# Kernel tuning notes

Hardware: AMD Instinct MI355X
Metric: run time of the kernel (lower is better)

The kernel has to match this reference:

```python
import jax, jax.numpy as jnp
import numpy as np

EPS = 1e-5
NEG_SLOPE = 0.2

def _layernorm(x, g, b):
    mu = x.mean(-1, keepdims=True)
    var = ((x - mu) ** 2).mean(-1, keepdims=True)
    return (x - mu) * jax.lax.rsqrt(var + EPS) * g + b

def _forward(h, edge_attr, rel_emb, W_l, b_l, W_r, b_r, W_e, att, bias, gate,
             g1, bt1, g2, bt2, Wf1, bf1, Wf2, bf2, edge_index, edge_type):
    N, F = h.shape
    R, H, C = att.shape
    HC = H * C
    E = edge_type.shape[0]
    De = edge_attr.shape[1]
    src, dst = edge_index[0], edge_index[1]

    # per-relation GATv2 linear projections: lin_l / lin_r  -> [N, R, H*C]
    xl = jnp.einsum('nf,rfh->nrh', h, W_l) + b_l
    xr = jnp.einsum('nf,rfh->nrh', h, W_r) + b_r
    # gather per edge using its own relation's weights
    xl_e = xl[src, edge_type]          # [E, HC]  (source, lin_l)
    xr_e = xr[dst, edge_type]          # [E, HC]  (dest,  lin_r)

    # edge features: lin_edge over concat([edge_attr, rel_emb[r]]) with per-relation weights
    e_feat = jnp.zeros((E, HC), dtype=h.dtype)
    for r in range(R):
        vr = edge_attr @ W_e[r, :De] + rel_emb[r] @ W_e[r, De:]  # [E,HC] + [HC]
        e_feat = jnp.where((edge_type == r)[:, None], vr, e_feat)

    # GATv2 attention score
    x = jax.nn.leaky_relu(xl_e + xr_e + e_feat, NEG_SLOPE).reshape(E, H, C)
    score = jnp.einsum('ehc,ehc->eh', x, att[edge_type])  # [E, H]

    # segment softmax per (destination node, relation)
    seg = dst * R + edge_type                              # [E]
    m = jax.lax.stop_gradient(jax.ops.segment_max(score, seg, num_segments=N * R))
    alpha = jnp.exp(score - m[seg])
    denom = jax.ops.segment_sum(alpha, seg, num_segments=N * R)
    alpha = alpha / denom[seg]                             # [E, H]

    # aggregate messages alpha * x_j (x_j = lin_l source features)
    msg = (xl_e.reshape(E, H, C) * alpha[..., None]).reshape(E, HC)
    agg = jax.ops.segment_sum(msg, seg, num_segments=N * R).reshape(N, R, H, C)
    h_rel = agg.mean(axis=2) + bias                        # concat=False -> head mean; [N, R, C]

    # learnable gated fusion over relations
    gw = jax.nn.softmax(gate)
    h_msg = jnp.einsum('r,nrc->nc', gw, h_rel)

    h1 = _layernorm(h + h_msg, g1, bt1)
    ffn = jax.nn.silu(h1 @ Wf1 + bf1) @ Wf2 + bf2
    return _layernorm(h1 + ffn, g2, bt2)


def setup_inputs() -> dict:
    key = jax.random.key(0)
    ks = jax.random.split(key, 16)
    N, F, E, De, Dr, R, H = 40000, 128, 150000, 16, 8, 4, 4
    C = F; HC = H * C; FFN = int(F * 2.0)
    s = 0.05
    return {
        'h': jax.random.normal(ks[0], (N, F), jnp.float32),
        'edge_index': jax.random.randint(ks[1], (2, E), 0, N),
        'edge_attr': jax.random.normal(ks[2], (E, De), jnp.float32),
        'edge_type': jax.random.randint(ks[3], (E,), 0, R),
        'rel_emb': jax.random.normal(ks[4], (R, Dr), jnp.float32) * s,
        'W_l': jax.random.normal(ks[5], (R, F, HC), jnp.float32) * s,
        'b_l': jnp.zeros((R, HC), jnp.float32),
        'W_r': jax.random.normal(ks[6], (R, F, HC), jnp.float32) * s,
        'b_r': jnp.zeros((R, HC), jnp.float32),
        'W_e': jax.random.normal(ks[7], (R, De + Dr, HC), jnp.float32) * s,
        'att': jax.random.normal(ks[8], (R, H, C), jnp.float32) * s,
        'bias': jnp.zeros((R, C), jnp.float32),
        'gate': jax.random.normal(ks[9], (R,), jnp.float32) * 0.5,
        'g1': jnp.ones((F,), jnp.float32), 'bt1': jnp.zeros((F,), jnp.float32),
        'g2': jnp.ones((F,), jnp.float32), 'bt2': jnp.zeros((F,), jnp.float32),
        'Wf1': jax.random.normal(ks[10], (F, FFN), jnp.float32) * s,
        'bf1': jnp.zeros((FFN,), jnp.float32),
        'Wf2': jax.random.normal(ks[11], (FFN, F), jnp.float32) * s,
        'bf2': jnp.zeros((F,), jnp.float32),
    }


def reference(h, edge_index, edge_attr, edge_type, rel_emb, W_l, b_l, W_r, b_r,
              W_e, att, bias, gate, g1, bt1, g2, bt2, Wf1, bf1, Wf2, bf2):
    return _forward(h, edge_attr, rel_emb, W_l, b_l, W_r, b_r, W_e, att, bias, gate,
                    g1, bt1, g2, bt2, Wf1, bf1, Wf2, bf2, edge_index, edge_type)
```

## Files before the change

### kernel.cpp

```cpp
#include <hip/hip_runtime.h>
#include <hip/hip_bf16.h>

#define NF   128
#define HCC  512
#define FFND 256
#define NEG  0.2f
#define EPSLN 1e-5f

typedef __attribute__((ext_vector_type(8))) short short8;
typedef __attribute__((ext_vector_type(4))) float f32x4;

__global__ void init_gw_kernel(const float* __restrict__ gate, float* __restrict__ gw) {
  if (threadIdx.x == 0 && blockIdx.x == 0) {
    float a = gate[0], b = gate[1], c = gate[2], d = gate[3];
    float m = fmaxf(fmaxf(a, b), fmaxf(c, d));
    float e0 = __expf(a - m), e1 = __expf(b - m), e2 = __expf(c - m), e3 = __expf(d - m);
    float s = e0 + e1 + e2 + e3;
    gw[0] = e0 / s; gw[1] = e1 / s; gw[2] = e2 / s; gw[3] = e3 / s;
  }
}

__global__ void init_all_kernel(float* __restrict__ denom, int* __restrict__ sorted,
                                int ndenom, int nsorted) {
  int i = blockIdx.x * 256 + threadIdx.x;
  if (i < ndenom)  denom[i] = 0.f;
  if (i < nsorted) sorted[i] = -1;
}

__global__ void init_hmsg_kernel(const float* __restrict__ gw, const float* __restrict__ bias,
                                 float* __restrict__ hmsg, int total) {
  int i = blockIdx.x * 256 + threadIdx.x;
  if (i < total) {
    int c = i & 127;
    hmsg[i] = gw[0]*bias[c] + gw[1]*bias[128+c] + gw[2]*bias[256+c] + gw[3]*bias[384+c];
  }
}

__global__ void transpose_bf16_kernel(const float* __restrict__ in, __hip_bfloat16* __restrict__ out,
                                      int rows, int cols, int total) {
  int i = blockIdx.x * 256 + threadIdx.x;
  if (i >= total) return;
  int per = rows * cols;
  int b = i / per, rem = i % per;
  int rr = rem / cols, cc = rem % cols;
  out[(size_t)b * per + (size_t)cc * rows + rr] = __float2bfloat16(in[i]);
}

__global__ void cvt_bf16_kernel(const float* __restrict__ in, __hip_bfloat16* __restrict__ out, int n) {
  int i4 = (blockIdx.x * 256 + threadIdx.x) * 4;
  if (i4 >= n) return;
  float4 v = *(const float4*)(in + i4);
  out[i4]     = __float2bfloat16(v.x);
  out[i4 + 1] = __float2bfloat16(v.y);
  out[i4 + 2] = __float2bfloat16(v.z);
  out[i4 + 3] = __float2bfloat16(v.w);
}

__global__ void prep_bias_kernel(const float* __restrict__ b_r, const float* __restrict__ rel_emb,
                                 const float* __restrict__ W_e, float* __restrict__ bias_comb) {
  int i = blockIdx.x * 256 + threadIdx.x;
  if (i >= 4 * 512) return;
  int col = i & 511, r = i >> 9;
  float v = b_r[i];
#pragma unroll
  for (int j = 0; j < 8; ++j)
    v += rel_emb[r * 8 + j] * W_e[(size_t)r * 24 * 512 + (size_t)(16 + j) * 512 + col];
  bias_comb[i] = v;
}

__global__ void blockhist_kernel(const int* __restrict__ etype, int* __restrict__ blockCnt, int E) {
  __shared__ int wcnt[4][4];
  int i = blockIdx.x * 256 + threadIdx.x;
  int rt = (i < E) ? etype[i] : -1;
  int wave = threadIdx.x >> 6, lane = threadIdx.x & 63;
#pragma unroll
  for (int r = 0; r < 4; ++r) {
    unsigned long long m = __ballot(rt == r);
    if (lane == 0) wcnt[wave][r] = __popcll(m);
  }
  __syncthreads();
  if (threadIdx.x < 4) {
    int r = threadIdx.x;
    blockCnt[blockIdx.x * 4 + r] = wcnt[0][r] + wcnt[1][r] + wcnt[2][r] + wcnt[3][r];
  }
}

__global__ void scan_kernel(const int* __restrict__ blockCnt, int* __restrict__ blockBase,
                            int* __restrict__ offs, int nBlocks) {
  __shared__ int lds[256];
  __shared__ int offs_s[5];
  __shared__ int tot_s[4];
  int t = threadIdx.x;
  int C = (nBlocks + 255) / 256;
  for (int r = 0; r < 4; ++r) {
    int s = 0;
    for (int b = t; b < nBlocks; b += 256) s += blockCnt[b * 4 + r];
    lds[t] = s;
    __syncthreads();
    for (int o = 128; o > 0; o >>= 1) {
      if (t < o) lds[t] += lds[t + o];
      __syncthreads();
    }
    if (t == 0) tot_s[r] = lds[0];
    __syncthreads();
  }
  if (t == 0) {
    int o = 0;
    offs_s[0] = 0;
    for (int r = 0; r < 4; ++r) { o += ((tot_s[r] + 63) >> 6) << 6; offs_s[r + 1] = o; }
    for (int r = 0; r < 5; ++r) offs[r] = offs_s[r];
  }
  __syncthreads();
  for (int r = 0; r < 4; ++r) {
    int b0 = t * C;
    int s = 0;
    for (int j = 0; j < C; ++j) {
      int b = b0 + j;
      if (b < nBlocks) s += blockCnt[b * 4 + r];
    }
    lds[t] = s;
    __syncthreads();
    int v = s;
    for (int o = 1; o < 256; o <<= 1) {
      int u = (t >= o) ? lds[t - o] : 0;
      __syncthreads();
      v += u;
      lds[t] = v;
      __syncthreads();
    }
    int run = offs_s[r] + (v - s);
    for (int j = 0; j < C; ++j) {
      int b = b0 + j;
      if (b < nBlocks) {
        blockBase[b * 4 + r] = run;
        run += blockCnt[b * 4 + r];
      }
    }
    __syncthreads();
  }
}

__global__ void scatter_kernel(const int* __restrict__ etype, const int* __restrict__ blockBase,
                               int* __restrict__ sorted, int E) {
  __shared__ int wcnt[4][4];
  int i = blockIdx.x * 256 + threadIdx.x;
  int rt = (i < E) ? etype[i] : -1;
  int wave = threadIdx.x >> 6, lane = threadIdx.x & 63;
  unsigned long long ltmask = (lane == 0) ? 0ull : (~0ull >> (64 - lane));
  int myrank = 0;
#pragma unroll
  for (int r = 0; r < 4; ++r) {
    unsigned long long m = __ballot(rt == r);
    if (lane == 0) wcnt[wave][r] = __popcll(m);
    if (rt == r) myrank = __popcll(m & ltmask);
  }
  __syncthreads();
  if (rt >= 0) {
    int wb = 0;
#pragma unroll
    for (int w = 0; w < 3; ++w) if (w < wave) wb += wcnt[w][rt];
    sorted[blockBase[blockIdx.x * 4 + rt] + wb + myrank] = i;
  }
}

__global__ __launch_bounds__(256) void proj_multi_kernel(
    const __hip_bfloat16* __restrict__ A,
    const __hip_bfloat16* __restrict__ Bt0, const float* __restrict__ bias0,
    __hip_bfloat16* __restrict__ out0,
    const __hip_bfloat16* __restrict__ Bt1, const float* __restrict__ bias1,
    __hip_bfloat16* __restrict__ out1,
    int M, int nch, int act)
{
  __shared__ __align__(16) short Bs[2][64 * 136];
  int side = blockIdx.y;
  const __hip_bfloat16* Bt = side ? Bt1 : Bt0;
  const float* bias = side ? bias1 : bias0;
  __hip_bfloat16* outp = side ? out1 : out0;
  int ldc = nch * 64;
  int tid = threadIdx.x;
  int rowBase = blockIdx.x * 128;
  int wid = tid >> 6, lane = tid & 63;
  int m16 = lane & 15, q = lane >> 4;

  short8 af[4][2];
#pragma unroll
  for (int mi = 0; mi < 2; ++mi) {
    int row = rowBase + wid * 32 + mi * 16 + m16;
    const __hip_bfloat16* ap = A + (size_t)row * 128 + q * 8;
    bool ok = row < M;
#pragma unroll
    for (int ks = 0; ks < 4; ++ks) {
      if (ok) af[ks][mi] = *(const short8*)(const void*)(ap + ks * 32);
      else { short8 z; for (int t = 0; t < 8; ++t) z[t] = 0; af[ks][mi] = z; }
    }
  }

#pragma unroll
  for (int t = 0; t < 4; ++t) {
    int c = tid + t * 256;
    int row = c >> 4, kk = (c & 15) << 3;
    *(short8*)(void*)(Bs[0] + row * 136 + kk) =
      *(const short8*)(const void*)(Bt + (size_t)row * 128 + kk);
  }
  __syncthreads();

  int p = 0;
  for (int cb = 0; cb < nch; ++cb) {
    int colBase = cb * 64;
    f32x4 acc[2][4];
#pragma unroll
    for (int mi = 0; mi < 2; ++mi)
#pragma unroll
      for (int ni = 0; ni < 4; ++ni) {
        acc[mi][ni][0] = 0.f; acc[mi][ni][1] = 0.f;
        acc[mi][ni][2] = 0.f; acc[mi][ni][3] = 0.f;
      }
#pragma unroll
    for (int ks = 0; ks < 4; ++ks) {
      int kof = (ks << 5) + (q << 3);
      short8 bfr[4];
#pragma unroll
      for (int ni = 0; ni < 4; ++ni)
        bfr[ni] = *(const short8*)(const void*)(Bs[p] + (ni * 16 + m16) * 136 + kof);
#pragma unroll
      for (int mi = 0; mi < 2; ++mi)
#pragma unroll
        for (int ni = 0; ni < 4; ++ni)
          acc[mi][ni] = __builtin_amdgcn_mfma_f32_16x16x32_bf16(bfr[ni], af[ks][mi], acc[mi][ni], 0, 0, 0);
    }
    if (cb + 1 < nch) {
#pragma unroll
      for (int t = 0; t < 4; ++t) {
        int c = tid + t * 256;
        int row = c >> 4, kk = (c & 15) << 3;
        *(short8*)(void*)(Bs[p ^ 1] + row * 136 + kk) =
          *(const short8*)(const void*)(Bt + (size_t)(colBase + 64 + row) * 128 + kk);
      }
    }
#pragma unroll
    for (int mi = 0; mi < 2; ++mi) {
      int row = rowBase + wid * 32 + mi * 16 + m16;
      if (row < M) {
#pragma unroll
        for (int ni = 0; ni < 4; ++ni) {
          int col0 = colBase + ni * 16 + q * 4;
          float4 b4 = *(const float4*)(bias + col0);
          float v0 = acc[mi][ni][0] + b4.x;
          float v1 = acc[mi][ni][1] + b4.y;
          float v2 = acc[mi][ni][2] + b4.z;
          float v3 = acc[mi][ni][3] + b4.w;
          if (act) {
            v0 = v0 / (1.f + __expf(-v0));
            v1 = v1 / (1.f + __expf(-v1));
            v2 = v2 / (1.f + __expf(-v2));
            v3 = v3 / (1.f + __expf(-v3));
          }
          __align__(8) __hip_bfloat16 tmp[4];
          tmp[0] = __float2bfloat16(v0);
          tmp[1] = __float2bfloat16(v1);
          tmp[2] = __float2bfloat16(v2);
          tmp[3] = __float2bfloat16(v3);
          *(uint2*)(void*)(outp + (size_t)row * ldc + col0) = *(const uint2*)(const void*)tmp;
        }
      }
    }
    __syncthreads();
    p ^= 1;
  }
}

__global__ __launch_bounds__(256) void mfma_gemm_kernel(
    const __hip_bfloat16* __restrict__ A,
    const __hip_bfloat16* __restrict__ Bt, const float* __restrict__ bias,
    float* __restrict__ Cout, int M, int K, int Ncols)
{
  __shared__ __align__(16) short Bs[64 * 136];
  int tid = threadIdx.x;
  int rowBase = blockIdx.y * 128, colBase = blockIdx.x * 64;
  int wid = tid >> 6, lane = tid & 63;
  int m16 = lane & 15, q = lane >> 4;

  f32x4 acc[2][4];
#pragma unroll
  for (int mi = 0; mi < 2; ++mi)
#pragma unroll
    for (int ni = 0; ni < 4; ++ni) {
      acc[mi][ni][0] = 0.f; acc[mi][ni][1] = 0.f;
      acc[mi][ni][2] = 0.f; acc[mi][ni][3] = 0.f;
    }

#pragma unroll 1
  for (int kc = 0; kc < K; kc += 128) {
#pragma unroll
    for (int t = 0; t < 4; ++t) {
      int c = tid + t * 256;
      int row = c >> 4, kk = (c & 15) << 3;
      *(short8*)(void*)(Bs + row * 136 + kk) =
        *(const short8*)(const void*)(Bt + (size_t)(colBase + row) * K + kc + kk);
    }
    __syncthreads();
    short8 af[4][2];
#pragma unroll
    for (int mi = 0; mi < 2; ++mi) {
      int row = rowBase + wid * 32 + mi * 16 + m16;
      const __hip_bfloat16* ap = A + (size_t)row * K + kc + q * 8;
      bool ok = row < M;
#pragma unroll
      for (int ks = 0; ks < 4; ++ks) {
        if (ok) af[ks][mi] = *(const short8*)(const void*)(ap + ks * 32);
        else { short8 z; for (int t2 = 0; t2 < 8; ++t2) z[t2] = 0; af[ks][mi] = z; }
      }
    }
#pragma unroll
    for (int ks = 0; ks < 4; ++ks) {
      int kof = (ks << 5) + (q << 3);
      short8 bfr[4];
#pragma unroll
      for (int ni = 0; ni < 4; ++ni)
        bfr[ni] = *(const short8*)(const void*)(Bs + (ni * 16 + m16) * 136 + kof);
#pragma unroll
      for (int mi = 0; mi < 2; ++mi)
#pragma unroll
        for (int ni = 0; ni < 4; ++ni)
          acc[mi][ni] = __builtin_amdgcn_mfma_f32_16x16x32_bf16(bfr[ni], af[ks][mi], acc[mi][ni], 0, 0, 0);
    }
    __syncthreads();
  }
#pragma unroll
  for (int mi = 0; mi < 2; ++mi) {
    int row = rowBase + wid * 32 + mi * 16 + m16;
    if (row < M) {
#pragma unroll
      for (int ni = 0; ni < 4; ++ni) {
        int col0 = colBase + ni * 16 + q * 4;
        float4 b4 = *(const float4*)(bias + col0);
        float4 v;
        v.x = acc[mi][ni][0] + b4.x;
        v.y = acc[mi][ni][1] + b4.y;
        v.z = acc[mi][ni][2] + b4.z;
        v.w = acc[mi][ni][3] + b4.w;
        *(float4*)(Cout + (size_t)row * Ncols + col0) = v;
      }
    }
  }
}

__global__ __launch_bounds__(256) void score_kernel(
    const int* __restrict__ sorted, const int* __restrict__ offs, int r,
    const int* __restrict__ eidx, const float* __restrict__ eattr,
    const float* __restrict__ W_e, const float* __restrict__ att,
    const __hip_bfloat16* __restrict__ xlr, const __hip_bfloat16* __restrict__ xrr,
    float* __restrict__ alpha, float* __restrict__ denom, int N, int E)
{
  __shared__ float We_s[16 * 512];
  __shared__ float att_s[512];
  int tid = threadIdx.x;
#pragma unroll
  for (int t = 0; t < 32; ++t) {
    int idx = tid + (t << 8);
    We_s[idx] = W_e[((size_t)r * 24 + (idx >> 9)) * 512 + (idx & 511)];
  }
  att_s[tid]       = att[r * 512 + tid];
  att_s[tid + 256] = att[r * 512 + tid + 256];
  __syncthreads();

  int base = offs[r], end = offs[r + 1];
  int lane = tid & 63;
  int head = lane >> 4;
  int wave = (blockIdx.x << 2) + (tid >> 6);
  int nw = gridDim.x << 2;
  float4 atv0 = *(const float4*)(att_s + lane * 8);
  float4 atv1 = *(const float4*)(att_s + lane * 8 + 4);

  for (int i = base + wave; i < end; i += nw) {
    int eid = sorted[i];
    if (eid < 0) continue;
    int src = eidx[eid], dst = eidx[E + eid];
    float4 a0 = *(const float4*)(eattr + (size_t)eid * 16);
    float4 a1 = *(const float4*)(eattr + (size_t)eid * 16 + 4);
    float4 a2 = *(const float4*)(eattr + (size_t)eid * 16 + 8);
    float4 a3 = *(const float4*)(eattr + (size_t)eid * 16 + 12);
    float4 lv = *(const float4*)(const void*)(xlr + (size_t)src * 512 + lane * 8);
    float4 rv = *(const float4*)(const void*)(xrr + (size_t)dst * 512 + lane * 8);
    const unsigned* lw = (const unsigned*)&lv;
    const unsigned* rw = (const unsigned*)&rv;
    float x[8];
#pragma unroll
    for (int j = 0; j < 4; ++j) {
      x[2*j]   = __uint_as_float(lw[j] << 16)         + __uint_as_float(rw[j] << 16);
      x[2*j+1] = __uint_as_float(lw[j] & 0xffff0000u) + __uint_as_float(rw[j] & 0xffff0000u);
    }
    float aa[16] = {a0.x,a0.y,a0.z,a0.w, a1.x,a1.y,a1.z,a1.w,
                    a2.x,a2.y,a2.z,a2.w, a3.x,a3.y,a3.z,a3.w};
    float ef[8] = {0.f,0.f,0.f,0.f,0.f,0.f,0.f,0.f};
#pragma unroll
    for (int k = 0; k < 16; ++k) {
      float4 w0 = *(const float4*)(We_s + k * 512 + lane * 8);
      float4 w1 = *(const float4*)(We_s + k * 512 + lane * 8 + 4);
      ef[0] += aa[k]*w0.x; ef[1] += aa[k]*w0.y; ef[2] += aa[k]*w0.z; ef[3] += aa[k]*w0.w;
      ef[4] += aa[k]*w1.x; ef[5] += aa[k]*w1.y; ef[6] += aa[k]*w1.z; ef[7] += aa[k]*w1.w;
    }
    const float* at = (const float*)&atv0;
    float s = 0.f;
#pragma unroll
    for (int j = 0; j < 8; ++j) {
      float xv = x[j] + ef[j];
      xv = (xv > 0.f) ? xv : NEG * xv;
      s += xv * ((j < 4) ? at[j] : ((const float*)&atv1)[j - 4]);
    }
    s += __shfl_xor(s, 1);
    s += __shfl_xor(s, 2);
    s += __shfl_xor(s, 4);
    s += __shfl_xor(s, 8);
    if ((lane & 15) == 0) {
      float al = __expf(s);
      alpha[(size_t)eid * 4 + head] = al;
      atomicAdd(&denom[((size_t)r * N + dst) * 4 + head], al);
    }
  }
}

__global__ __launch_bounds__(256) void agg_kernel(
    const int* __restrict__ sorted, const int* __restrict__ offs, int r,
    const int* __restrict__ eidx, const float* __restrict__ alpha,
    const float* __restrict__ denom, const __hip_bfloat16* __restrict__ xlr,
    const float* __restrict__ gw, float* __restrict__ hmsg, int N, int E)
{
  int base = offs[r], end = offs[r + 1];
  float g = 0.25f * gw[r];
  int lane = threadIdx.x & 63;
  int wave = (blockIdx.x << 2) + (threadIdx.x >> 6);
  int nw = gridDim.x << 2;
  int col = lane * 2;
  for (int i = base + wave; i < end; i += nw) {
    int eid = sorted[i];
    if (eid < 0) continue;
    int src = eidx[eid], dst = eidx[E + eid];
    float4 al = *(const float4*)(alpha + (size_t)eid * 4);
    float4 dn = *(const float4*)(denom + ((size_t)r * N + dst) * 4);
    float coef[4] = {g * al.x / dn.x, g * al.y / dn.y, g * al.z / dn.z, g * al.w / dn.w};
    float s0 = 0.f, s1 = 0.f;
#pragma unroll
    for (int hh = 0; hh < 4; ++hh) {
      unsigned pw = *(const unsigned*)(const void*)(xlr + (size_t)src * 512 + hh * 128 + col);
      s0 += coef[hh] * __uint_as_float(pw << 16);
      s1 += coef[hh] * __uint_as_float(pw & 0xffff0000u);
    }
    atomicAdd(&hmsg[(size_t)dst * 128 + col],     s0);
    atomicAdd(&hmsg[(size_t)dst * 128 + col + 1], s1);
  }
}

__global__ __launch_bounds__(256) void ln_kernel(
    const float* __restrict__ X, const float* __restrict__ Y,
    const float* __restrict__ g, const float* __restrict__ b,
    float* __restrict__ out, __hip_bfloat16* __restrict__ outbf, int N)
{
  int w = (int)((blockIdx.x * (unsigned)blockDim.x + threadIdx.x) >> 6);
  int lane = threadIdx.x & 63;
  if (w >= N) return;
  int c = lane * 2;
  float2 xv = *(const float2*)(X + (size_t)w * 128 + c);
  float2 yv = *(const float2*)(Y + (size_t)w * 128 + c);
  float v0 = xv.x + yv.x, v1 = xv.y + yv.y;
  float s1 = v0 + v1, s2 = v0 * v0 + v1 * v1;
#pragma unroll
  for (int off = 1; off < 64; off <<= 1) {
    s1 += __shfl_xor(s1, off);
    s2 += __shfl_xor(s2, off);
  }
  float mu = s1 * (1.f / 128.f);
  float var = s2 * (1.f / 128.f) - mu * mu;
  float rstd = rsqrtf(var + EPSLN);
  float o0 = (v0 - mu) * rstd * g[c]     + b[c];
  float o1 = (v1 - mu) * rstd * g[c + 1] + b[c + 1];
  out[(size_t)w * 128 + c]     = o0;
  out[(size_t)w * 128 + c + 1] = o1;
  if (outbf) {
    outbf[(size_t)w * 128 + c]     = __float2bfloat16(o0);
    outbf[(size_t)w * 128 + c + 1] = __float2bfloat16(o1);
  }
}

extern "C" void kernel_launch(void* const* d_in, const int* in_sizes, int n_in,
                              void* d_out, int out_size, void* d_ws, size_t ws_size,
                              hipStream_t stream) {
  const float* h       = (const float*)d_in[0];
  const int*   eidx    = (const int*)d_in[1];
  const float* eattr   = (const float*)d_in[2];
  const int*   etype   = (const int*)d_in[3];
  const float* rel_emb = (const float*)d_in[4];
  const float* W_l     = (const float*)d_in[5];
  const float* b_l     = (const float*)d_in[6];
  const float* W_r     = (const float*)d_in[7];
  const float* b_r     = (const float*)d_in[8];
  const float* W_e     = (const float*)d_in[9];
  const float* att     = (const float*)d_in[10];
  const float* bias    = (const float*)d_in[11];
  const float* gate    = (const float*)d_in[12];
  const float* g1      = (const float*)d_in[13];
  const float* bt1     = (const float*)d_in[14];
  const float* g2      = (const float*)d_in[15];
  const float* bt2     = (const float*)d_in[16];
  const float* Wf1     = (const float*)d_in[17];
  const float* bf1     = (const float*)d_in[18];
  const float* Wf2     = (const float*)d_in[19];
  const float* bf2     = (const float*)d_in[20];

  const int N = in_sizes[0] / NF;
  const int E = in_sizes[3];
  const int nTiles = (E + 4 * 63 + 63) / 64;
  const int sortedN = nTiles * 64;
  const int Mtiles = (N + 127) / 128;
  const int histBlocks = (E + 255) / 256;

  char* ws = (char*)d_ws;
  size_t off = 0;
  auto carve = [&](size_t bytes) -> void* {
    void* p = ws + off;
    off = (off + bytes + 255) & ~(size_t)255;
    return p;
  };
  __hip_bfloat16* xl_r  = (__hip_bfloat16*)carve((size_t)N * 512 * 2);
  __hip_bfloat16* xr_r  = (__hip_bfloat16*)carve((size_t)N * 512 * 2);
  __hip_bfloat16* hbf   = (__hip_bfloat16*)carve((size_t)N * 128 * 2);
  __hip_bfloat16* Wlt   = (__hip_bfloat16*)carve((size_t)4 * 512 * 128 * 2);
  __hip_bfloat16* Wrt   = (__hip_bfloat16*)carve((size_t)4 * 512 * 128 * 2);
  __hip_bfloat16* Wf1t  = (__hip_bfloat16*)carve((size_t)256 * 128 * 2);
  __hip_bfloat16* Wf2t  = (__hip_bfloat16*)carve((size_t)128 * 256 * 2);
  float*    bias_c = (float*)carve((size_t)4 * 512 * 4);
  float*    alpha  = (float*)carve((size_t)E * 4 * 4);
  float*    denom  = (float*)carve((size_t)4 * N * 4 * 4);
  float*    hmsg   = (float*)carve((size_t)N * 128 * 4);
  int*      sorted = (int*)carve((size_t)sortedN * 4);
  int*      blockCnt  = (int*)carve((size_t)histBlocks * 4 * 4);
  int*      blockBase = (int*)carve((size_t)histBlocks * 4 * 4);
  int*      offsb  = (int*)carve(64);
  float*    gw     = (float*)carve(256);
  float*          h1   = (float*)(ws + 0);
  __hip_bfloat16* h1bf = (__hip_bfloat16*)(ws + (size_t)N * 128 * 4);
  __hip_bfloat16* uffn = (__hip_bfloat16*)(ws + (size_t)N * 128 * 6);
  float*          yffn = (float*)(ws + (size_t)N * 128 * 6 + (size_t)N * 256 * 2);
  float*          out  = (float*)d_out;

  init_gw_kernel<<<1, 64, 0, stream>>>(gate, gw);
  {
    int ndenom = 4 * N * 4;
    int mx = (ndenom > sortedN) ? ndenom : sortedN;
    init_all_kernel<<<(mx + 255) / 256, 256, 0, stream>>>(denom, sorted, ndenom, sortedN);
  }
  init_hmsg_kernel<<<(N * 128 + 255) / 256, 256, 0, stream>>>(gw, bias, hmsg, N * 128);
  cvt_bf16_kernel<<<(N * 128 / 4 + 255) / 256, 256, 0, stream>>>(h, hbf, N * 128);
  transpose_bf16_kernel<<<(4 * 128 * 512 + 255) / 256, 256, 0, stream>>>(W_l, Wlt, 128, 512, 4 * 128 * 512);
  transpose_bf16_kernel<<<(4 * 128 * 512 + 255) / 256, 256, 0, stream>>>(W_r, Wrt, 128, 512, 4 * 128 * 512);
  transpose_bf16_kernel<<<(128 * 256 + 255) / 256, 256, 0, stream>>>(Wf1, Wf1t, 128, 256, 128 * 256);
  transpose_bf16_kernel<<<(256 * 128 + 255) / 256, 256, 0, stream>>>(Wf2, Wf2t, 256, 128, 256 * 128);
  prep_bias_kernel<<<(4 * 512 + 255) / 256, 256, 0, stream>>>(b_r, rel_emb, W_e, bias_c);
  blockhist_kernel<<<histBlocks, 256, 0, stream>>>(etype, blockCnt, E);
  scan_kernel<<<1, 256, 0, stream>>>(blockCnt, blockBase, offsb, histBlocks);
  scatter_kernel<<<histBlocks, 256, 0, stream>>>(etype, blockBase, sorted, E);

  for (int r = 0; r < 4; ++r) {
    proj_multi_kernel<<<dim3(Mtiles, 2), 256, 0, stream>>>(
        hbf,
        Wlt + (size_t)r * 512 * 128, b_l + r * 512, xl_r,
        Wrt + (size_t)r * 512 * 128, bias_c + r * 512, xr_r,
        N, 8, 0);
    score_kernel<<<1024, 256, 0, stream>>>(sorted, offsb, r, eidx, eattr, W_e, att,
                                           xl_r, xr_r, alpha, denom, N, E);
    agg_kernel<<<1024, 256, 0, stream>>>(sorted, offsb, r, eidx, alpha, denom,
                                         xl_r, gw, hmsg, N, E);
  }

  ln_kernel<<<(N + 3) / 4, 256, 0, stream>>>(h, hmsg, g1, bt1, h1, h1bf, N);
  proj_multi_kernel<<<dim3(Mtiles, 1), 256, 0, stream>>>(
      h1bf, Wf1t, bf1, uffn, Wf1t, bf1, uffn, N, 4, 1);
  mfma_gemm_kernel<<<dim3(NF / 64, Mtiles), 256, 0, stream>>>(
      uffn, Wf2t, bf2, yffn, N, 256, NF);
  ln_kernel<<<(N + 3) / 4, 256, 0, stream>>>(h1, yffn, g2, bt2, out, nullptr, N);
}
```

Baseline: 630.8 us.

## Merge setup kernels into one prep kernel and split projection columns across grid z

Nine small setup launches (gate softmax, zero-init, hmsg init, bf16 conversion, weight transposes, bias prep) become a single grid-stride kernel, removing launch gaps. The projection GEMM also gains a z grid dimension that splits the output column chunks in half, doubling the block count for more parallelism. In exchange, each block reloads its A fragments, and every thread recomputes the gate softmax. The fused transpose writes are still uncoalesced.

```diff
diff --git a/kernel.cpp b/kernel.cpp
--- a/kernel.cpp
+++ b/kernel.cpp
@@ -10,62 +10,72 @@
 typedef __attribute__((ext_vector_type(8))) short short8;
 typedef __attribute__((ext_vector_type(4))) float f32x4;
 
-__global__ void init_gw_kernel(const float* __restrict__ gate, float* __restrict__ gw) {
-  if (threadIdx.x == 0 && blockIdx.x == 0) {
-    float a = gate[0], b = gate[1], c = gate[2], d = gate[3];
-    float m = fmaxf(fmaxf(a, b), fmaxf(c, d));
-    float e0 = __expf(a - m), e1 = __expf(b - m), e2 = __expf(c - m), e3 = __expf(d - m);
-    float s = e0 + e1 + e2 + e3;
-    gw[0] = e0 / s; gw[1] = e1 / s; gw[2] = e2 / s; gw[3] = e3 / s;
-  }
-}
-
-__global__ void init_all_kernel(float* __restrict__ denom, int* __restrict__ sorted,
-                                int ndenom, int nsorted) {
-  int i = blockIdx.x * 256 + threadIdx.x;
-  if (i < ndenom)  denom[i] = 0.f;
-  if (i < nsorted) sorted[i] = -1;
-}
-
-__global__ void init_hmsg_kernel(const float* __restrict__ gw, const float* __restrict__ bias,
-                                 float* __restrict__ hmsg, int total) {
-  int i = blockIdx.x * 256 + threadIdx.x;
-  if (i < total) {
-    int c = i & 127;
-    hmsg[i] = gw[0]*bias[c] + gw[1]*bias[128+c] + gw[2]*bias[256+c] + gw[3]*bias[384+c];
-  }
-}
-
-__global__ void transpose_bf16_kernel(const float* __restrict__ in, __hip_bfloat16* __restrict__ out,
-                                      int rows, int cols, int total) {
-  int i = blockIdx.x * 256 + threadIdx.x;
-  if (i >= total) return;
-  int per = rows * cols;
-  int b = i / per, rem = i % per;
-  int rr = rem / cols, cc = rem % cols;
-  out[(size_t)b * per + (size_t)cc * rows + rr] = __float2bfloat16(in[i]);
-}
-
-__global__ void cvt_bf16_kernel(const float* __restrict__ in, __hip_bfloat16* __restrict__ out, int n) {
-  int i4 = (blockIdx.x * 256 + threadIdx.x) * 4;
-  if (i4 >= n) return;
-  float4 v = *(const float4*)(in + i4);
-  out[i4]     = __float2bfloat16(v.x);
-  out[i4 + 1] = __float2bfloat16(v.y);
-  out[i4 + 2] = __float2bfloat16(v.z);
-  out[i4 + 3] = __float2bfloat16(v.w);
-}
-
-__global__ void prep_bias_kernel(const float* __restrict__ b_r, const float* __restrict__ rel_emb,
-                                 const float* __restrict__ W_e, float* __restrict__ bias_comb) {
-  int i = blockIdx.x * 256 + threadIdx.x;
-  if (i >= 4 * 512) return;
-  int col = i & 511, r = i >> 9;
-  float v = b_r[i];
-#pragma unroll
-  for (int j = 0; j < 8; ++j)
-    v += rel_emb[r * 8 + j] * W_e[(size_t)r * 24 * 512 + (size_t)(16 + j) * 512 + col];
-  bias_comb[i] = v;
+__global__ void prep_all_kernel(
+    const float* __restrict__ h, __hip_bfloat16* __restrict__ hbf,
+    const float* __restrict__ W_l, __hip_bfloat16* __restrict__ Wlt,
+    const float* __restrict__ W_r, __hip_bfloat16* __restrict__ Wrt,
+    const float* __restrict__ Wf1, __hip_bfloat16* __restrict__ Wf1t,
+    const float* __restrict__ Wf2, __hip_bfloat16* __restrict__ Wf2t,
+    const float* __restrict__ b_r, const float* __restrict__ rel_emb,
+    const float* __restrict__ W_e, float* __restrict__ bias_c,
+    const float* __restrict__ gate, float* __restrict__ gw,
+    const float* __restrict__ bias, float* __restrict__ hmsg,
+    float* __restrict__ denom, int* __restrict__ sorted,
+    int N, int sortedN)
+{
+  int tid0 = blockIdx.x * 256 + threadIdx.x;
+  int stride = gridDim.x * 256;
+  float a0 = gate[0], a1 = gate[1], a2 = gate[2], a3 = gate[3];
+  float mx = fmaxf(fmaxf(a0, a1), fmaxf(a2, a3));
+  float e0 = __expf(a0 - mx), e1 = __expf(a1 - mx), e2 = __expf(a2 - mx), e3 = __expf(a3 - mx);
+  float inv = 1.f / (e0 + e1 + e2 + e3);
+  float g0 = e0 * inv, g1 = e1 * inv, g2 = e2 * inv, g3 = e3 * inv;
+  if (tid0 == 0) { gw[0] = g0; gw[1] = g1; gw[2] = g2; gw[3] = g3; }
+  for (int i = tid0; i < N * 32; i += stride) {
+    float4 v = ((const float4*)h)[i];
+    __align__(8) __hip_bfloat16 t[4] = {
+      __float2bfloat16(v.x), __float2bfloat16(v.y),
+      __float2bfloat16(v.z), __float2bfloat16(v.w)};
+    ((uint2*)hbf)[i] = *(const uint2*)(const void*)t;
+  }
+  for (int i = tid0; i < 4 * 128 * 512; i += stride) {
+    int col = i & 511, row = (i >> 9) & 127, b = i >> 16;
+    size_t o = ((size_t)b << 16) + ((size_t)col << 7) + row;
+    Wlt[o] = __float2bfloat16(W_l[i]);
+    Wrt[o] = __float2bfloat16(W_r[i]);
+  }
+  for (int i = tid0; i < 128 * 256; i += stride) {
+    int col = i & 255, row = i >> 8;
+    Wf1t[col * 128 + row] = __float2bfloat16(Wf1[i]);
+  }
+  for (int i = tid0; i < 256 * 128; i += stride) {
+    int col = i & 127, row = i >> 7;
+    Wf2t[col * 256 + row] = __float2bfloat16(Wf2[i]);
+  }
+  for (int i = tid0; i < 4 * 512; i += stride) {
+    int col = i & 511, r = i >> 9;
+    float v = b_r[i];
+#pragma unroll
+    for (int j = 0; j < 8; ++j)
+      v += rel_emb[r * 8 + j] * W_e[((size_t)r * 24 + 16 + j) * 512 + col];
+    bias_c[i] = v;
+  }
+  for (int i = tid0; i < N * 4; i += stride)
+    ((float4*)denom)[i] = make_float4(0.f, 0.f, 0.f, 0.f);
+  for (int i = tid0; i < sortedN; i += stride) sorted[i] = -1;
+  for (int i = tid0; i < N * 32; i += stride) {
+    int c = (i & 31) * 4;
+    float4 b0 = *(const float4*)(bias + c);
+    float4 b1 = *(const float4*)(bias + 128 + c);
+    float4 b2 = *(const float4*)(bias + 256 + c);
+    float4 b3 = *(const float4*)(bias + 384 + c);
+    float4 o;
+    o.x = g0 * b0.x + g1 * b1.x + g2 * b2.x + g3 * b3.x;
+    o.y = g0 * b0.y + g1 * b1.y + g2 * b2.y + g3 * b3.y;
+    o.z = g0 * b0.z + g1 * b1.z + g2 * b2.z + g3 * b3.z;
+    o.w = g0 * b0.w + g1 * b1.w + g2 * b2.w + g3 * b3.w;
+    ((float4*)hmsg)[i] = o;
+  }
 }
 
 __global__ void blockhist_kernel(const int* __restrict__ etype, int* __restrict__ blockCnt, int E) {
@@ -169,14 +179,14 @@
     __hip_bfloat16* __restrict__ out0,
     const __hip_bfloat16* __restrict__ Bt1, const float* __restrict__ bias1,
     __hip_bfloat16* __restrict__ out1,
-    int M, int nch, int act)
+    int M, int ldc, int nchPer, int act)
 {
   __shared__ __align__(16) short Bs[2][64 * 136];
   int side = blockIdx.y;
   const __hip_bfloat16* Bt = side ? Bt1 : Bt0;
   const float* bias = side ? bias1 : bias0;
   __hip_bfloat16* outp = side ? out1 : out0;
-  int ldc = nch * 64;
+  int cb0 = blockIdx.z * nchPer;
   int tid = threadIdx.x;
   int rowBase = blockIdx.x * 128;
   int wid = tid >> 6, lane = tid & 63;
@@ -200,12 +210,12 @@
     int c = tid + t * 256;
     int row = c >> 4, kk = (c & 15) << 3;
     *(short8*)(void*)(Bs[0] + row * 136 + kk) =
-      *(const short8*)(const void*)(Bt + (size_t)row * 128 + kk);
+      *(const short8*)(const void*)(Bt + (size_t)(cb0 * 64 + row) * 128 + kk);
   }
   __syncthreads();
 
   int p = 0;
-  for (int cb = 0; cb < nch; ++cb) {
+  for (int cb = cb0; cb < cb0 + nchPer; ++cb) {
     int colBase = cb * 64;
     f32x4 acc[2][4];
 #pragma unroll
@@ -228,7 +238,7 @@
         for (int ni = 0; ni < 4; ++ni)
           acc[mi][ni] = __builtin_amdgcn_mfma_f32_16x16x32_bf16(bfr[ni], af[ks][mi], acc[mi][ni], 0, 0, 0);
     }
-    if (cb + 1 < nch) {
+    if (cb + 1 < cb0 + nchPer) {
 #pragma unroll
       for (int t = 0; t < 4; ++t) {
         int c = tid + t * 256;
@@ -543,29 +553,19 @@
   float*          yffn = (float*)(ws + (size_t)N * 128 * 6 + (size_t)N * 256 * 2);
   float*          out  = (float*)d_out;
 
-  init_gw_kernel<<<1, 64, 0, stream>>>(gate, gw);
-  {
-    int ndenom = 4 * N * 4;
-    int mx = (ndenom > sortedN) ? ndenom : sortedN;
-    init_all_kernel<<<(mx + 255) / 256, 256, 0, stream>>>(denom, sorted, ndenom, sortedN);
-  }
-  init_hmsg_kernel<<<(N * 128 + 255) / 256, 256, 0, stream>>>(gw, bias, hmsg, N * 128);
-  cvt_bf16_kernel<<<(N * 128 / 4 + 255) / 256, 256, 0, stream>>>(h, hbf, N * 128);
-  transpose_bf16_kernel<<<(4 * 128 * 512 + 255) / 256, 256, 0, stream>>>(W_l, Wlt, 128, 512, 4 * 128 * 512);
-  transpose_bf16_kernel<<<(4 * 128 * 512 + 255) / 256, 256, 0, stream>>>(W_r, Wrt, 128, 512, 4 * 128 * 512);
-  transpose_bf16_kernel<<<(128 * 256 + 255) / 256, 256, 0, stream>>>(Wf1, Wf1t, 128, 256, 128 * 256);
-  transpose_bf16_kernel<<<(256 * 128 + 255) / 256, 256, 0, stream>>>(Wf2, Wf2t, 256, 128, 256 * 128);
-  prep_bias_kernel<<<(4 * 512 + 255) / 256, 256, 0, stream>>>(b_r, rel_emb, W_e, bias_c);
+  prep_all_kernel<<<1024, 256, 0, stream>>>(
+      h, hbf, W_l, Wlt, W_r, Wrt, Wf1, Wf1t, Wf2, Wf2t,
+      b_r, rel_emb, W_e, bias_c, gate, gw, bias, hmsg, denom, sorted, N, sortedN);
   blockhist_kernel<<<histBlocks, 256, 0, stream>>>(etype, blockCnt, E);
   scan_kernel<<<1, 256, 0, stream>>>(blockCnt, blockBase, offsb, histBlocks);
   scatter_kernel<<<histBlocks, 256, 0, stream>>>(etype, blockBase, sorted, E);
 
   for (int r = 0; r < 4; ++r) {
-    proj_multi_kernel<<<dim3(Mtiles, 2), 256, 0, stream>>>(
+    proj_multi_kernel<<<dim3(Mtiles, 2, 2), 256, 0, stream>>>(
         hbf,
         Wlt + (size_t)r * 512 * 128, b_l + r * 512, xl_r,
         Wrt + (size_t)r * 512 * 128, bias_c + r * 512, xr_r,
-        N, 8, 0);
+        N, 512, 4, 0);
     score_kernel<<<1024, 256, 0, stream>>>(sorted, offsb, r, eidx, eattr, W_e, att,
                                            xl_r, xr_r, alpha, denom, N, E);
     agg_kernel<<<1024, 256, 0, stream>>>(sorted, offsb, r, eidx, alpha, denom,
@@ -573,8 +573,8 @@
   }
 
   ln_kernel<<<(N + 3) / 4, 256, 0, stream>>>(h, hmsg, g1, bt1, h1, h1bf, N);
-  proj_multi_kernel<<<dim3(Mtiles, 1), 256, 0, stream>>>(
-      h1bf, Wf1t, bf1, uffn, Wf1t, bf1, uffn, N, 4, 1);
+  proj_multi_kernel<<<dim3(Mtiles, 1, 2), 256, 0, stream>>>(
+      h1bf, Wf1t, bf1, uffn, Wf1t, bf1, uffn, N, 256, 2, 1);
   mfma_gemm_kernel<<<dim3(NF / 64, Mtiles), 256, 0, stream>>>(
       uffn, Wf2t, bf2, yffn, N, 256, NF);
   ln_kernel<<<(N + 3) / 4, 256, 0, stream>>>(h1, yffn, g2, bt2, out, nullptr, N);
```

New measurement: 613.5 us. 2.7% less time.
